# Performance work log

Measured on AMD Instinct MI355X. Metric: run time of the kernel, lower is better.

Reference implementation:

```python
import jax, jax.numpy as jnp
import numpy as np

C_Z = 128
C_H = 128
N = 512
B = 1

def _layer_norm(x, g, b, eps=1e-5):
    mu = jnp.mean(x, axis=-1, keepdims=True)
    var = jnp.var(x, axis=-1, keepdims=True)
    return (x - mu) * jax.lax.rsqrt(var + eps) * g + b

def _linear(x, w, b):
    # torch Linear: y = x @ w.T + b, w: [out, in]
    return jnp.einsum('...i,oi->...o', x, w) + b

def setup_inputs() -> dict:
    key = jax.random.key(0)
    ks = jax.random.split(key, 8)
    s = 1.0 / np.sqrt(C_Z)
    return {
        'z': jax.random.normal(ks[0], (B, N, N, C_Z), jnp.float32),
        'mask': jnp.ones((B, N, N), jnp.float32),
        'ln_in_g': jnp.ones((C_Z,), jnp.float32),
        'ln_in_b': jnp.zeros((C_Z,), jnp.float32),
        'w_ag': jax.random.normal(ks[1], (C_H, C_Z), jnp.float32) * s,
        'b_ag': jnp.ones((C_H,), jnp.float32),
        'w_ap': jax.random.normal(ks[2], (C_H, C_Z), jnp.float32) * s,
        'b_ap': jnp.zeros((C_H,), jnp.float32),
        'w_bg': jax.random.normal(ks[3], (C_H, C_Z), jnp.float32) * s,
        'b_bg': jnp.ones((C_H,), jnp.float32),
        'w_bp': jax.random.normal(ks[4], (C_H, C_Z), jnp.float32) * s,
        'b_bp': jnp.zeros((C_H,), jnp.float32),
        'w_g': jax.random.normal(ks[5], (C_Z, C_Z), jnp.float32) * s,
        'b_g': jnp.zeros((C_Z,), jnp.float32),
        'w_z': jax.random.normal(ks[6], (C_Z, C_H), jnp.float32) * s,
        'b_z': jnp.zeros((C_Z,), jnp.float32),
        'ln_out_g': jnp.ones((C_H,), jnp.float32),
        'ln_out_b': jnp.zeros((C_H,), jnp.float32),
    }

def reference(z, mask, ln_in_g, ln_in_b, w_ag, b_ag, w_ap, b_ap,
              w_bg, b_bg, w_bp, b_bp, w_g, b_g, w_z, b_z,
              ln_out_g, ln_out_b):
    m = mask[..., None]                       # [B,N,N,1]
    zn = _layer_norm(z, ln_in_g, ln_in_b)     # [B,N,N,Cz]
    a = m * jax.nn.sigmoid(_linear(zn, w_ag, b_ag)) * _linear(zn, w_ap, b_ap)
    b = m * jax.nn.sigmoid(_linear(zn, w_bg, b_bg)) * _linear(zn, w_bp, b_bp)
    # outgoing: x[b,i,j,c] = sum_k a[b,i,k,c] * b[b,j,k,c]
    x = jnp.einsum('bikc,bjkc->bijc', a, b)
    x = _layer_norm(x, ln_out_g, ln_out_b)
    x = _linear(x, w_z, b_z)
    g = jax.nn.sigmoid(_linear(zn, w_g, b_g))
    return x * g
```

## Files before the change

### kernel.cpp

```cpp
#include <hip/hip_runtime.h>

#define NN 512
#define CCH 128
#define MM (NN*NN)

using f32x4  = __attribute__((ext_vector_type(4))) float;
using f32x2  = __attribute__((ext_vector_type(2))) float;
using bf16x8 = __attribute__((ext_vector_type(8))) short;
using u16x4  = __attribute__((ext_vector_type(4))) unsigned short;
using u32x2  = __attribute__((ext_vector_type(2))) unsigned int;
using u32x4  = __attribute__((ext_vector_type(4))) unsigned int;
typedef unsigned short u16;

__device__ __forceinline__ u16 f2bf(float f) {
    unsigned u = __builtin_bit_cast(unsigned, f);
    u += 0x7FFF + ((u >> 16) & 1);
    return (u16)(u >> 16);
}
__device__ __forceinline__ float bf2f(u16 h) {
    unsigned u = ((unsigned)h) << 16;
    return __builtin_bit_cast(float, u);
}
__device__ __forceinline__ unsigned pack2(float lo, float hi) {
    return (unsigned)f2bf(lo) | ((unsigned)f2bf(hi) << 16);
}
__device__ __forceinline__ float sigm(float x) { return 1.0f / (1.0f + __expf(-x)); }

__device__ __forceinline__ void gl_lds16(const void* g, void* l) {
    __builtin_amdgcn_global_load_lds(
        (const __attribute__((address_space(1))) void*)g,
        (__attribute__((address_space(3))) void*)l, 16, 0, 0);
}

__global__ __launch_bounds__(256) void k_prep(
    const float* __restrict__ w0, const float* __restrict__ w1,
    const float* __restrict__ w2, const float* __restrict__ w3,
    const float* __restrict__ w4, const float* __restrict__ w5,
    const float* __restrict__ b0, const float* __restrict__ b1,
    const float* __restrict__ b2, const float* __restrict__ b3,
    const float* __restrict__ b4, const float* __restrict__ b5,
    const float* __restrict__ gin, const float* __restrict__ bin,
    const float* __restrict__ gout, const float* __restrict__ bout,
    u16* __restrict__ wbf, float* __restrict__ bias2) {
    int mat = blockIdx.x;
    const float* W = mat==0?w0:mat==1?w1:mat==2?w2:mat==3?w3:mat==4?w4:w5;
    const float* B = mat==0?b0:mat==1?b1:mat==2?b2:mat==3?b3:mat==4?b4:b5;
    const float* G = (mat==5)? gout : gin;
    const float* Bt= (mat==5)? bout : bin;
    __shared__ float gs[CCH], bs[CCH];
    int tid = threadIdx.x;
    if (tid < CCH) { gs[tid] = G[tid]; bs[tid] = Bt[tid]; }
    __syncthreads();
    int o = tid >> 1, c0 = (tid & 1) * 64;
    const float* src = W + o * CCH + c0;
    char* dstrow = (char*)(wbf + mat * 16384) + o * 256;
    int key = o & 7;
    float dot = 0.f;
    #pragma unroll
    for (int q = 0; q < 16; ++q) {
        f32x4 v = *(const f32x4*)(src + q * 4);
        int c = c0 + q * 4;
        dot += bs[c]*v.x + bs[c+1]*v.y + bs[c+2]*v.z + bs[c+3]*v.w;
        u16x4 p;
        p.x = f2bf(v.x * gs[c]);     p.y = f2bf(v.y * gs[c+1]);
        p.z = f2bf(v.z * gs[c+2]);   p.w = f2bf(v.w * gs[c+3]);
        int chunk = (c0 >> 3) + (q >> 1);
        *(u16x4*)(dstrow + (((chunk ^ key)) << 4) + ((q & 1) << 3)) = p;
    }
    dot += __shfl_xor(dot, 1);
    if ((tid & 1) == 0) bias2[mat * CCH + o] = B[o] + dot;
}

__global__ __launch_bounds__(256) void k_fused(
    const float* __restrict__ z, const float* __restrict__ mask,
    const u16* __restrict__ wbf, const float* __restrict__ bias2,
    u16* __restrict__ aT, u16* __restrict__ bT, u16* gateB) {
    __shared__ __align__(16) u16 znt[8192];
    __shared__ __align__(16) u16 wls[32768];
    int tid = threadIdx.x, w = tid >> 6, lane = tid & 63;
    int r = lane & 15, kq = lane >> 4;
    long m0 = (long)blockIdx.x * 64;

    {
        const char* Wg = (const char*)wbf;
        #pragma unroll
        for (int it = 0; it < 16; ++it)
            gl_lds16(Wg + (long)it * 4096 + tid * 16, (char*)wls + it * 4096 + w * 1024);
    }

    {
        int row = tid >> 2, p = tid & 3, c0 = p * 32;
        const float* zr = z + (m0 + row) * CCH + c0;
        f32x4 va[8];
        float s = 0.f, s2 = 0.f;
        #pragma unroll
        for (int q = 0; q < 8; ++q) {
            va[q] = *(const f32x4*)(zr + q * 4);
            s  += va[q].x + va[q].y + va[q].z + va[q].w;
            s2 += va[q].x*va[q].x + va[q].y*va[q].y + va[q].z*va[q].z + va[q].w*va[q].w;
        }
        s += __shfl_xor(s, 1);  s += __shfl_xor(s, 2);
        s2 += __shfl_xor(s2, 1); s2 += __shfl_xor(s2, 2);
        float mu = s * (1.0f / CCH);
        float var = fmaxf(s2 * (1.0f / CCH) - mu * mu, 0.f);
        float rs = rsqrtf(var + 1e-5f);
        int sw = (row & 15) << 4;
        #pragma unroll
        for (int q2 = 0; q2 < 4; ++q2) {
            f32x4 v0 = va[q2*2], v1 = va[q2*2+1];
            u32x2 pk;
            pk.x = pack2((v0.x-mu)*rs, (v0.y-mu)*rs);
            pk.y = pack2((v0.z-mu)*rs, (v0.w-mu)*rs);
            u32x2 pk2;
            pk2.x = pack2((v1.x-mu)*rs, (v1.y-mu)*rs);
            pk2.y = pack2((v1.z-mu)*rs, (v1.w-mu)*rs);
            char* p8 = (char*)znt + row * 256 + ((c0 * 2 + q2 * 16) ^ sw);
            *(u32x2*)p8 = pk;
            *(u32x2*)(p8 + 8) = pk2;
        }
    }
    __syncthreads();

    bf16x8 av[4];
    {
        int row = w * 16 + r, sw = (row & 15) << 4;
        #pragma unroll
        for (int kb = 0; kb < 4; ++kb)
            av[kb] = *(const bf16x8*)((const char*)znt + row * 256 + ((kb * 64 + kq * 16) ^ sw));
    }
    f32x4 mkv = *(const f32x4*)(mask + m0 + w * 16 + kq * 4);

    int i7 = (int)((blockIdx.x >> 3) & 7);
    int qch = w * 2 + (kq >> 1);
    long boff = m0 * 2 + (long)((qch ^ i7) << 4) + ((kq & 1) << 3);

    #pragma unroll 1
    for (int ph = 0; ph < 2; ++ph) {
        if (ph == 1) {
            __syncthreads();
            const char* Wg = (const char*)wbf + 65536;
            #pragma unroll
            for (int it = 0; it < 16; ++it)
                gl_lds16(Wg + (long)it * 4096 + tid * 16, (char*)wls + it * 4096 + w * 1024);
            __syncthreads();
        }
        const float* B1 = bias2 + (ph * 2) * CCH;
        const float* B2 = bias2 + (ph * 2 + 1) * CCH;
        f32x4 acc1[8], acc2[8];
        #pragma unroll
        for (int nt = 0; nt < 8; ++nt) { acc1[nt] = {0,0,0,0}; acc2[nt] = {0,0,0,0}; }
        #pragma unroll
        for (int nt = 0; nt < 8; ++nt) {
            int ol = nt * 16 + r;
            int key = ol & 7;
            const char* row1 = (const char*)wls + ol * 256;
            const char* row2 = (const char*)wls + 32768 + ol * 256;
            #pragma unroll
            for (int kb = 0; kb < 4; ++kb) {
                int ph16 = ((kb * 4 + kq) ^ key) << 4;
                bf16x8 b1 = *(const bf16x8*)(row1 + ph16);
                bf16x8 b2 = *(const bf16x8*)(row2 + ph16);
                acc1[nt] = __builtin_amdgcn_mfma_f32_16x16x32_bf16(av[kb], b1, acc1[nt], 0, 0, 0);
                acc2[nt] = __builtin_amdgcn_mfma_f32_16x16x32_bf16(av[kb], b2, acc2[nt], 0, 0, 0);
            }
        }
        u16* dst = ph ? bT : aT;
        #pragma unroll
        for (int nt = 0; nt < 8; ++nt) {
            int cc = nt * 16 + r;
            float b1v = B1[cc], b2v = B2[cc];
            float v0 = mkv[0] * sigm(acc1[nt][0] + b1v) * (acc2[nt][0] + b2v);
            float v1 = mkv[1] * sigm(acc1[nt][1] + b1v) * (acc2[nt][1] + b2v);
            float v2 = mkv[2] * sigm(acc1[nt][2] + b1v) * (acc2[nt][2] + b2v);
            float v3 = mkv[3] * sigm(acc1[nt][3] + b1v) * (acc2[nt][3] + b2v);
            u32x2 pv; pv.x = pack2(v0, v1); pv.y = pack2(v2, v3);
            *(u32x2*)((char*)dst + ((long)cc << 19) + boff) = pv;
        }
    }

    __syncthreads();
    {
        const char* Wg = (const char*)wbf + 131072;
        #pragma unroll
        for (int it = 0; it < 8; ++it)
            gl_lds16(Wg + (long)it * 4096 + tid * 16, (char*)wls + it * 4096 + w * 1024);
    }
    __syncthreads();
    {
        f32x4 acc[8];
        #pragma unroll
        for (int nt = 0; nt < 8; ++nt) acc[nt] = {0,0,0,0};
        #pragma unroll
        for (int nt = 0; nt < 8; ++nt) {
            int ol = nt * 16 + r;
            int key = ol & 7;
            const char* row1 = (const char*)wls + ol * 256;
            #pragma unroll
            for (int kb = 0; kb < 4; ++kb) {
                bf16x8 b1 = *(const bf16x8*)(row1 + (((kb * 4 + kq) ^ key) << 4));
                acc[nt] = __builtin_amdgcn_mfma_f32_16x16x32_bf16(b1, av[kb], acc[nt], 0, 0, 0);
            }
        }
        long m = m0 + w * 16 + r;
        #pragma unroll
        for (int nt = 0; nt < 8; ++nt) {
            int c0 = nt * 16 + kq * 4;
            f32x4 bg = *(const f32x4*)(bias2 + 4 * CCH + c0);
            u32x2 pv;
            pv.x = pack2(sigm(acc[nt][0] + bg[0]), sigm(acc[nt][1] + bg[1]));
            pv.y = pack2(sigm(acc[nt][2] + bg[2]), sigm(acc[nt][3] + bg[3]));
            *(u32x2*)(gateB + m * 256 + c0) = pv;
        }
    }
}

__global__ __launch_bounds__(256, 4) void k_tri(const u16* __restrict__ aT,
                                                const u16* __restrict__ bT,
                                                u16* __restrict__ xT) {
    __shared__ __align__(16) char shm[34816];
    u16* At = (u16*)shm;
    u16* Bt = (u16*)(shm + 16384);
    int tid = threadIdx.x;
    int w = tid >> 6, lane = tid & 63;
    int r = lane & 15, kq = lane >> 4;

    int L = blockIdx.x;
    int xcd = L & 7, idx = L >> 3;
    int c    = xcd + 8 * (idx >> 4);
    int tile = idx & 15;
    int ti = tile >> 2, tj = tile & 3;

    const char* abase = (const char*)(aT + (long)c * MM) + (long)(ti * 128) * 1024;
    const char* bbase = (const char*)(bT + (long)c * MM) + (long)(tj * 128) * 1024;
    int wm = w >> 1, wn = w & 1;

    f32x4 acc[4][4];
    #pragma unroll
    for (int a = 0; a < 4; ++a)
        #pragma unroll
        for (int bq = 0; bq < 4; ++bq) acc[a][bq] = {0.f,0.f,0.f,0.f};

    for (int ks = 0; ks < 8; ++ks) {
        const char* asrc = abase + ks * 128;
        const char* bsrc = bbase + ks * 128;
        #pragma unroll
        for (int it = 0; it < 4; ++it) {
            int u = it * 256 + tid;
            long goff = (long)(u >> 3) * 1024 + (u & 7) * 16;
            gl_lds16(asrc + goff, (char*)At + it * 4096 + w * 1024);
            gl_lds16(bsrc + goff, (char*)Bt + it * 4096 + w * 1024);
        }
        __syncthreads();

        #pragma unroll
        for (int kh = 0; kh < 2; ++kh) {
            bf16x8 af[4];
            #pragma unroll
            for (int mt = 0; mt < 4; ++mt) {
                int rowa = wm * 64 + mt * 16 + r;
                af[mt] = *(const bf16x8*)((const char*)At + rowa * 128 +
                                          (((kh * 4 + kq) ^ (r & 7)) << 4));
            }
            #pragma unroll
            for (int nt = 0; nt < 4; ++nt) {
                int rowb = wn * 64 + nt * 16 + r;
                bf16x8 bf = *(const bf16x8*)((const char*)Bt + rowb * 128 +
                                             (((kh * 4 + kq) ^ (r & 7)) << 4));
                #pragma unroll
                for (int mt = 0; mt < 4; ++mt)
                    acc[mt][nt] = __builtin_amdgcn_mfma_f32_16x16x32_bf16(bf, af[mt], acc[mt][nt], 0, 0, 0);
            }
        }
        __syncthreads();
    }

    char* tb = shm;
    #pragma unroll
    for (int mt = 0; mt < 4; ++mt) {
        int il = wm * 64 + mt * 16 + r;
        #pragma unroll
        for (int nt = 0; nt < 4; ++nt) {
            int jl = wn * 64 + nt * 16 + kq * 4;
            u32x2 pv;
            pv.x = pack2(acc[mt][nt][0], acc[mt][nt][1]);
            pv.y = pack2(acc[mt][nt][2], acc[mt][nt][3]);
            *(u32x2*)(tb + il * 272 + jl * 2) = pv;
        }
    }
    __syncthreads();
    u16* xrow = xT + (long)c * MM + (long)(ti * 128) * NN + tj * 128;
    int joff = tid & 15;
    #pragma unroll
    for (int rd = 0; rd < 8; ++rd) {
        int il = rd * 16 + (tid >> 4);
        u32x4 vv = *(const u32x4*)(tb + il * 272 + joff * 16);
        *(u32x4*)(xrow + (long)il * NN + joff * 8) = vv;
    }
}

__global__ __launch_bounds__(256, 4) void k_out(const u16* __restrict__ xT,
                                                const u16* __restrict__ wbf,
                                                const float* __restrict__ bias2,
                                                const u16* gateB,
                                                float* __restrict__ outp) {
    __shared__ __align__(16) u16 xl[64 * 128];
    int tid = threadIdx.x, w = tid >> 6, lane = tid & 63;
    int r = lane & 15, kq = lane >> 4;
    long m0 = (long)blockIdx.x * 64;

    {
        int cg = tid & 31, ms = tid >> 5;
        int c0 = cg * 4;
        const u16* base = xT + m0 + (long)ms * 8;
        bf16x8 v0 = *(const bf16x8*)(base + (long)(c0 + 0) * MM);
        bf16x8 v1 = *(const bf16x8*)(base + (long)(c0 + 1) * MM);
        bf16x8 v2 = *(const bf16x8*)(base + (long)(c0 + 2) * MM);
        bf16x8 v3 = *(const bf16x8*)(base + (long)(c0 + 3) * MM);
        #pragma unroll
        for (int e = 0; e < 8; ++e) {
            int m = ms * 8 + e;
            u16x4 t;
            t.x = (u16)v0[e]; t.y = (u16)v1[e]; t.z = (u16)v2[e]; t.w = (u16)v3[e];
            *(u16x4*)((char*)xl + m * 256 + ((c0 * 2) ^ ((m & 15) << 4))) = t;
        }
    }
    __syncthreads();

    int mlr = w * 16 + r;
    int swm = (mlr & 15) << 4;
    u32x4 avu[4];
    float s = 0.f, s2 = 0.f;
    #pragma unroll
    for (int kb = 0; kb < 4; ++kb) {
        avu[kb] = *(const u32x4*)((const char*)xl + mlr * 256 + ((kb * 64 + kq * 16) ^ swm));
        #pragma unroll
        for (int p = 0; p < 4; ++p) {
            unsigned u = avu[kb][p];
            float flo = __builtin_bit_cast(float, u << 16);
            float fhi = __builtin_bit_cast(float, u & 0xFFFF0000u);
            s += flo + fhi;
            s2 = fmaf(flo, flo, s2);
            s2 = fmaf(fhi, fhi, s2);
        }
    }
    s  += __shfl_xor(s, 16);  s  += __shfl_xor(s, 32);
    s2 += __shfl_xor(s2, 16); s2 += __shfl_xor(s2, 32);
    float mu = s * (1.0f / CCH);
    float var = fmaxf(s2 * (1.0f / CCH) - mu * mu, 0.f);
    float rs = rsqrtf(var + 1e-5f);
    float nmu = -mu * rs;
    bf16x8 av[4];
    #pragma unroll
    for (int kb = 0; kb < 4; ++kb) {
        u32x4 o;
        #pragma unroll
        for (int p = 0; p < 4; ++p) {
            unsigned u = avu[kb][p];
            float flo = __builtin_bit_cast(float, u << 16);
            float fhi = __builtin_bit_cast(float, u & 0xFFFF0000u);
            o[p] = pack2(fmaf(flo, rs, nmu), fmaf(fhi, rs, nmu));
        }
        av[kb] = __builtin_bit_cast(bf16x8, o);
    }

    long m = m0 + w * 16 + r;
    u16x4 gvu[8];
    #pragma unroll
    for (int nt = 0; nt < 8; ++nt)
        gvu[nt] = *(const u16x4*)(gateB + m * 256 + nt * 16 + kq * 4);

    const char* Wz = (const char*)(wbf + 5 * 16384);
    f32x4 acc[8];
    #pragma unroll
    for (int nt = 0; nt < 8; ++nt) acc[nt] = {0,0,0,0};
    #pragma unroll
    for (int nt = 0; nt < 8; ++nt) {
        int ol = nt * 16 + r;
        int key = ol & 7;
        const char* row = Wz + ol * 256;
        #pragma unroll
        for (int kb = 0; kb < 4; ++kb) {
            bf16x8 bw = *(const bf16x8*)(row + (((kb * 4 + kq) ^ key) << 4));
            acc[nt] = __builtin_amdgcn_mfma_f32_16x16x32_bf16(bw, av[kb], acc[nt], 0, 0, 0);
        }
    }

    __syncthreads();

    const float* b2z = bias2 + 5 * CCH;
    #pragma unroll
    for (int nt = 0; nt < 8; ++nt) {
        int c0 = nt * 16 + kq * 4;
        f32x4 bb = *(const f32x4*)(b2z + c0);
        f32x4 o;
        #pragma unroll
        for (int j = 0; j < 4; ++j)
            o[j] = (acc[nt][j] + bb[j]) * bf2f(gvu[nt][j]);
        *(f32x4*)(outp + m * CCH + c0) = o;
    }
}

extern "C" void kernel_launch(void* const* d_in, const int* in_sizes, int n_in,
                              void* d_out, int out_size, void* d_ws, size_t ws_size,
                              hipStream_t stream) {
    const float* z       = (const float*)d_in[0];
    const float* mask    = (const float*)d_in[1];
    const float* ln_in_g = (const float*)d_in[2];
    const float* ln_in_b = (const float*)d_in[3];
    const float* w_ag    = (const float*)d_in[4];
    const float* b_ag    = (const float*)d_in[5];
    const float* w_ap    = (const float*)d_in[6];
    const float* b_ap    = (const float*)d_in[7];
    const float* w_bg    = (const float*)d_in[8];
    const float* b_bg    = (const float*)d_in[9];
    const float* w_bp    = (const float*)d_in[10];
    const float* b_bp    = (const float*)d_in[11];
    const float* w_g     = (const float*)d_in[12];
    const float* b_g     = (const float*)d_in[13];
    const float* w_z     = (const float*)d_in[14];
    const float* b_z     = (const float*)d_in[15];
    const float* ln_o_g  = (const float*)d_in[16];
    const float* ln_o_b  = (const float*)d_in[17];
    float* out = (float*)d_out;
    u16* gateB = (u16*)d_out;

    char* ws = (char*)d_ws;
    const size_t SL = (size_t)MM * CCH * 2;
    u16* xT   = (u16*)ws;
    u16* aT   = (u16*)(ws + SL);
    u16* bT   = (u16*)(ws + 2 * SL);
    u16* wbf  = (u16*)(ws + 3 * SL);
    float* b2 = (float*)(ws + 3 * SL + 6 * 16384 * 2);

    k_prep<<<6, 256, 0, stream>>>(w_ag, w_ap, w_bg, w_bp, w_g, w_z,
                                  b_ag, b_ap, b_bg, b_bp, b_g, b_z,
                                  ln_in_g, ln_in_b, ln_o_g, ln_o_b, wbf, b2);
    k_fused<<<MM / 64, 256, 0, stream>>>(z, mask, wbf, b2, aT, bT, gateB);
    k_tri<<<2048, 256, 0, stream>>>(aT, bT, xT);
    k_out<<<MM / 64, 256, 0, stream>>>(xT, wbf, b2, gateB, out);
}
```

Baseline: 316.8 us.

## Double k_fused block to 128 rows and load z directly into MFMA operand registers

k_fused now runs 512 threads per block over 128 rows, so each staged weight tile in LDS is shared by twice as many rows and the weight loads are amortised. The input LayerNorm no longer goes through an LDS transpose buffer. Each lane loads its own MFMA fragment of z from global memory, reduces the row statistics with cross-lane shuffles, and packs the bf16 operands straight into registers, removing the znt buffer and one barrier. The aT/bT output swizzle is adjusted for the larger block. The risks are a less coalesced z read pattern, higher register pressure under the new launch bounds, and half as many blocks in the grid.

```diff
diff --git a/kernel.cpp b/kernel.cpp
--- a/kernel.cpp
+++ b/kernel.cpp
@@ -71,68 +71,63 @@
     if ((tid & 1) == 0) bias2[mat * CCH + o] = B[o] + dot;
 }
 
-__global__ __launch_bounds__(256) void k_fused(
+__global__ __launch_bounds__(512, 4) void k_fused(
     const float* __restrict__ z, const float* __restrict__ mask,
     const u16* __restrict__ wbf, const float* __restrict__ bias2,
     u16* __restrict__ aT, u16* __restrict__ bT, u16* gateB) {
-    __shared__ __align__(16) u16 znt[8192];
     __shared__ __align__(16) u16 wls[32768];
     int tid = threadIdx.x, w = tid >> 6, lane = tid & 63;
     int r = lane & 15, kq = lane >> 4;
-    long m0 = (long)blockIdx.x * 64;
+    long m0 = (long)blockIdx.x * 128;
 
     {
         const char* Wg = (const char*)wbf;
         #pragma unroll
-        for (int it = 0; it < 16; ++it)
-            gl_lds16(Wg + (long)it * 4096 + tid * 16, (char*)wls + it * 4096 + w * 1024);
-    }
-
+        for (int it = 0; it < 8; ++it)
+            gl_lds16(Wg + (long)it * 8192 + tid * 16, (char*)wls + it * 8192 + w * 1024);
+    }
+
+    long mrow = m0 + w * 16 + r;
+    bf16x8 av[4];
     {
-        int row = tid >> 2, p = tid & 3, c0 = p * 32;
-        const float* zr = z + (m0 + row) * CCH + c0;
-        f32x4 va[8];
+        const float* zr = z + mrow * CCH;
+        f32x4 zv[4][2];
         float s = 0.f, s2 = 0.f;
         #pragma unroll
-        for (int q = 0; q < 8; ++q) {
-            va[q] = *(const f32x4*)(zr + q * 4);
-            s  += va[q].x + va[q].y + va[q].z + va[q].w;
-            s2 += va[q].x*va[q].x + va[q].y*va[q].y + va[q].z*va[q].z + va[q].w*va[q].w;
-        }
-        s += __shfl_xor(s, 1);  s += __shfl_xor(s, 2);
-        s2 += __shfl_xor(s2, 1); s2 += __shfl_xor(s2, 2);
+        for (int kb = 0; kb < 4; ++kb) {
+            zv[kb][0] = *(const f32x4*)(zr + kb * 32 + kq * 8);
+            zv[kb][1] = *(const f32x4*)(zr + kb * 32 + kq * 8 + 4);
+            #pragma unroll
+            for (int h = 0; h < 2; ++h) {
+                f32x4 v = zv[kb][h];
+                s += v.x + v.y + v.z + v.w;
+                s2 = fmaf(v.x, v.x, fmaf(v.y, v.y, fmaf(v.z, v.z, fmaf(v.w, v.w, s2))));
+            }
+        }
+        s  += __shfl_xor(s, 16);  s  += __shfl_xor(s, 32);
+        s2 += __shfl_xor(s2, 16); s2 += __shfl_xor(s2, 32);
         float mu = s * (1.0f / CCH);
         float var = fmaxf(s2 * (1.0f / CCH) - mu * mu, 0.f);
         float rs = rsqrtf(var + 1e-5f);
-        int sw = (row & 15) << 4;
-        #pragma unroll
-        for (int q2 = 0; q2 < 4; ++q2) {
-            f32x4 v0 = va[q2*2], v1 = va[q2*2+1];
-            u32x2 pk;
-            pk.x = pack2((v0.x-mu)*rs, (v0.y-mu)*rs);
-            pk.y = pack2((v0.z-mu)*rs, (v0.w-mu)*rs);
-            u32x2 pk2;
-            pk2.x = pack2((v1.x-mu)*rs, (v1.y-mu)*rs);
-            pk2.y = pack2((v1.z-mu)*rs, (v1.w-mu)*rs);
-            char* p8 = (char*)znt + row * 256 + ((c0 * 2 + q2 * 16) ^ sw);
-            *(u32x2*)p8 = pk;
-            *(u32x2*)(p8 + 8) = pk2;
-        }
-    }
-    __syncthreads();
-
-    bf16x8 av[4];
-    {
-        int row = w * 16 + r, sw = (row & 15) << 4;
-        #pragma unroll
-        for (int kb = 0; kb < 4; ++kb)
-            av[kb] = *(const bf16x8*)((const char*)znt + row * 256 + ((kb * 64 + kq * 16) ^ sw));
+        #pragma unroll
+        for (int kb = 0; kb < 4; ++kb) {
+            f32x4 a0 = zv[kb][0], a1 = zv[kb][1];
+            u32x4 o;
+            o[0] = pack2((a0.x - mu) * rs, (a0.y - mu) * rs);
+            o[1] = pack2((a0.z - mu) * rs, (a0.w - mu) * rs);
+            o[2] = pack2((a1.x - mu) * rs, (a1.y - mu) * rs);
+            o[3] = pack2((a1.z - mu) * rs, (a1.w - mu) * rs);
+            av[kb] = __builtin_bit_cast(bf16x8, o);
+        }
     }
     f32x4 mkv = *(const f32x4*)(mask + m0 + w * 16 + kq * 4);
 
-    int i7 = (int)((blockIdx.x >> 3) & 7);
-    int qch = w * 2 + (kq >> 1);
-    long boff = m0 * 2 + (long)((qch ^ i7) << 4) + ((kq & 1) << 3);
+    __syncthreads();
+
+    int i7 = (int)((blockIdx.x >> 2) & 7);
+    int q = w * 2 + (kq >> 1);
+    long boff = m0 * 2 + ((long)(q >> 3) << 7) + ((long)((q & 7) ^ i7) << 4)
+              + ((kq & 1) << 3);
 
     #pragma unroll 1
     for (int ph = 0; ph < 2; ++ph) {
@@ -140,8 +135,8 @@
             __syncthreads();
             const char* Wg = (const char*)wbf + 65536;
             #pragma unroll
-            for (int it = 0; it < 16; ++it)
-                gl_lds16(Wg + (long)it * 4096 + tid * 16, (char*)wls + it * 4096 + w * 1024);
+            for (int it = 0; it < 8; ++it)
+                gl_lds16(Wg + (long)it * 8192 + tid * 16, (char*)wls + it * 8192 + w * 1024);
             __syncthreads();
         }
         const float* B1 = bias2 + (ph * 2) * CCH;
@@ -182,8 +177,8 @@
     {
         const char* Wg = (const char*)wbf + 131072;
         #pragma unroll
-        for (int it = 0; it < 8; ++it)
-            gl_lds16(Wg + (long)it * 4096 + tid * 16, (char*)wls + it * 4096 + w * 1024);
+        for (int it = 0; it < 4; ++it)
+            gl_lds16(Wg + (long)it * 8192 + tid * 16, (char*)wls + it * 8192 + w * 1024);
     }
     __syncthreads();
     {
@@ -201,7 +196,6 @@
                 acc[nt] = __builtin_amdgcn_mfma_f32_16x16x32_bf16(b1, av[kb], acc[nt], 0, 0, 0);
             }
         }
-        long m = m0 + w * 16 + r;
         #pragma unroll
         for (int nt = 0; nt < 8; ++nt) {
             int c0 = nt * 16 + kq * 4;
@@ -209,7 +203,7 @@
             u32x2 pv;
             pv.x = pack2(sigm(acc[nt][0] + bg[0]), sigm(acc[nt][1] + bg[1]));
             pv.y = pack2(sigm(acc[nt][2] + bg[2]), sigm(acc[nt][3] + bg[3]));
-            *(u32x2*)(gateB + m * 256 + c0) = pv;
+            *(u32x2*)(gateB + mrow * 256 + c0) = pv;
         }
     }
 }
@@ -435,7 +429,7 @@
     k_prep<<<6, 256, 0, stream>>>(w_ag, w_ap, w_bg, w_bp, w_g, w_z,
                                   b_ag, b_ap, b_bg, b_bp, b_g, b_z,
                                   ln_in_g, ln_in_b, ln_o_g, ln_o_b, wbf, b2);
-    k_fused<<<MM / 64, 256, 0, stream>>>(z, mask, wbf, b2, aT, bT, gateB);
+    k_fused<<<MM / 128, 512, 0, stream>>>(z, mask, wbf, b2, aT, bT, gateB);
     k_tri<<<2048, 256, 0, stream>>>(aT, bT, xT);
     k_out<<<MM / 64, 256, 0, stream>>>(xT, wbf, b2, gateB, out);
 }
```

Result: no change. 311.3 us (-1.7%).
